# Performance work log

Hardware: AMD Instinct MI355X
Metric: run time of the kernel (lower is better)

## Reference

```python
import jax, jax.numpy as jnp
from jax import lax
import numpy as np

B = 2048
NUM_COMPO = 650
NUM_CHARS = 27533
COMPO_SCORE_THRESH = 0.7
SCORE_ADJ_SCALE = 0.1
K = 10  # top-k chars and max padded hit indices


def setup_inputs() -> dict:
    key = jax.random.key(0)
    k1, k2, k3, k4, k5 = jax.random.split(key, 5)
    return {
        "pred_class_logits": jax.random.normal(k1, (B, NUM_CHARS), dtype=jnp.float32),
        "pred_compo_logits": jax.random.normal(k2, (B, NUM_COMPO), dtype=jnp.float32),
        "chinese_char_ids": jax.random.randint(k3, (B,), 0, NUM_CHARS, dtype=jnp.int32),
        "compo_co_occurrence_prob": jax.random.uniform(k4, (NUM_COMPO, NUM_COMPO), dtype=jnp.float32),
        "compo_chinese_matrix": jax.random.randint(k5, (NUM_COMPO, NUM_CHARS), 0, 2, dtype=jnp.int32),
    }


def _components_to_char(compo_scores, co_occ, matrix):
    """Per-sample: compo_scores [C], co_occ [C,C], matrix [C,V] (0/1 int)."""
    # score adjustment: sum over compos with score>0.88 of co_occ row * score * scale
    hi = compo_scores > 0.88
    w = jnp.where(hi, compo_scores, 0.0)                       # [C]
    adjusted = compo_scores + SCORE_ADJ_SCALE * (w @ co_occ)   # [C]
    max_idx = jnp.argmax(adjusted)
    max_score = compo_scores[max_idx]

    # select compos above threshold, sorted descending by score
    sel = compo_scores > COMPO_SCORE_THRESH
    num_sel = jnp.sum(sel.astype(jnp.int32))
    masked = jnp.where(sel, compo_scores, -jnp.inf)
    order = jnp.argsort(-masked)                                # selected first, desc
    sorted_scores = jnp.take(compo_scores, order)               # [C]

    hit0 = matrix[max_idx]                                      # [V] int

    def cond(st):
        i, hit, _prev = st
        return (i < num_sel) & (jnp.sum(hit) > 1)

    def body(st):
        i, hit, _prev = st
        comp = matrix[order[i]]
        new_hit = ((hit + comp) == 2).astype(hit.dtype)         # intersection
        return (i + 1, new_hit, hit)

    i, hit, prev = lax.while_loop(cond, body, (jnp.int32(1), hit0, hit0))
    num_hit = jnp.sum(hit)
    empty = num_hit == 0
    i = jnp.where(empty, i - 1, i)
    hit = jnp.where(empty, prev, hit)
    hit_score = jnp.where(i == 1, max_score, sorted_scores[i - 1])

    # first K indices where hit == 1, padded with -1 (fixed shape)
    ar = jnp.arange(NUM_CHARS, dtype=jnp.int32)
    vals = jnp.where(hit == 1, NUM_CHARS - ar, 0)
    topv, topi = lax.top_k(vals, K)
    hit_indices = jnp.where(topv > 0, topi.astype(jnp.int32), -1)
    return adjusted, hit_indices, hit_score


def reference(pred_class_logits, pred_compo_logits, chinese_char_ids,
              compo_co_occurrence_prob, compo_chinese_matrix):
    class_probs = jax.nn.softmax(pred_class_logits, axis=1)     # [B, V]
    compo_scores = jax.nn.sigmoid(pred_compo_logits)            # [B, C]
    class_scores, class_indices = lax.top_k(class_probs, K)     # [B, K]

    adjusted, hit_idx, hit_scores = jax.vmap(
        _components_to_char, in_axes=(0, None, None)
    )(compo_scores, compo_co_occurrence_prob, compo_chinese_matrix)

    num_hit = jnp.sum((hit_idx != -1).astype(jnp.int32), axis=1)  # [B]
    pred1 = jnp.where(num_hit == 1, hit_idx[:, 0], class_indices[:, 0])
    pred2 = jnp.where((class_scores[:, 0] < 0.85) & (num_hit == 1),
                      hit_idx[:, 0], class_indices[:, 0])

    hit_compare = jnp.any(class_indices[:, :, None] == hit_idx[:, None, :], axis=2)  # [B,K]
    j = jnp.argmax(hit_compare, axis=1)  # first True (all-False -> 0), matches stable desc argsort[0]
    pred3 = class_indices[jnp.arange(class_indices.shape[0]), j]

    return (class_indices, class_scores, compo_scores, adjusted,
            hit_idx, hit_scores, pred1, pred2, pred3)
```

## Files before the change

kernel.cpp:

```cpp
#include <hip/hip_runtime.h>
#include <math.h>

#define NB 2048
#define NC 650
#define NV 27533
#define NK 10
#define NWRD 861
#define NT 256
#define NCHUNK 11
#define SVCAP 768
#define T0 2.5f

__global__ __launch_bounds__(NT) void pack_kernel(const int* __restrict__ mat,
                                                  unsigned* __restrict__ packed) {
  const int c = blockIdx.x;
  __shared__ unsigned s_w[NWRD];
  for (int w = threadIdx.x; w < NWRD; w += NT) s_w[w] = 0;
  __syncthreads();
  const size_t rbeg = (size_t)c * NV;
  const size_t g0 = rbeg & ~(size_t)3;
  const int pre = (int)(rbeg - g0);
  const int nchunks = (NV + pre + 3) >> 2;
  const size_t NTOT = (size_t)NC * NV;
  for (int t = threadIdx.x; t < nchunks; t += NT) {
    size_t g = g0 + ((size_t)t << 2);
    int4 q;
    if (g + 4 <= NTOT) {
      q = *(const int4*)(mat + g);
    } else {
      q.x = (g < NTOT) ? mat[g] : 0;
      q.y = (g + 1 < NTOT) ? mat[g + 1] : 0;
      q.z = (g + 2 < NTOT) ? mat[g + 2] : 0;
      q.w = (g + 3 < NTOT) ? mat[g + 3] : 0;
    }
    long e0 = (long)g - (long)rbeg;
    unsigned nib = 0;
    if (q.x && e0 >= 0 && e0 < NV) nib |= 1u;
    if (q.y && e0 + 1 >= 0 && e0 + 1 < NV) nib |= 2u;
    if (q.z && e0 + 2 >= 0 && e0 + 2 < NV) nib |= 4u;
    if (q.w && e0 + 3 >= 0 && e0 + 3 < NV) nib |= 8u;
    if (nib) {
      if (e0 < 0) { nib >>= (int)(-e0); e0 = 0; }
      int w = (int)(e0 >> 5), sh = (int)(e0 & 31);
      unsigned long long m = (unsigned long long)nib << sh;
      atomicOr(&s_w[w], (unsigned)m);
      unsigned hi = (unsigned)(m >> 32);
      if (hi && w + 1 < NWRD) atomicOr(&s_w[w + 1], hi);
    }
  }
  __syncthreads();
  unsigned* orow = packed + (size_t)c * NWRD;
  for (int w = threadIdx.x; w < NWRD; w += NT) orow[w] = s_w[w];
}

__global__ __launch_bounds__(NT, 6) void gen_pred_kernel(
    const float* __restrict__ class_logits,
    const float* __restrict__ compo_logits,
    const float* __restrict__ co_occ,
    const unsigned* __restrict__ packed,
    float* __restrict__ out) {
  const int b = blockIdx.x;
  const int tid = threadIdx.x;
  const int lane = tid & 63;
  const int wid = tid >> 6;

  __shared__ __align__(16) char arena[10464];
  float* s_sv_v = (float*)arena;
  int* s_sv_i = (int*)(arena + 3072);
  float* s_score = (float*)arena;
  int* s_selidx = (int*)(arena + 2608);
  int* s_hi = (int*)(arena + 5216);
  int* s_order = (int*)(arena + 7824);
  __shared__ unsigned s_words[NWRD];

  __shared__ float red_f[4];
  __shared__ float red_s[4];
  __shared__ int red_i[4];
  __shared__ int s_svcnt, s_cnt, s_i;
  __shared__ int s_cls_idx[NK];
  __shared__ float s_cls_sc[NK];
  __shared__ int s_hit[NK];
  __shared__ int s_hicnt[NCHUNK];
  __shared__ int s_selcnt[NCHUNK];

  const size_t o_cidx = 0;
  const size_t o_csc = (size_t)NB * NK;
  const size_t o_comp = 2 * (size_t)NB * NK;
  const size_t o_adj = o_comp + (size_t)NB * NC;
  const size_t o_hidx = o_adj + (size_t)NB * NC;
  const size_t o_hsc = o_hidx + (size_t)NB * NK;
  const size_t o_p1 = o_hsc + NB;
  const size_t o_p2 = o_p1 + NB;
  const size_t o_p3 = o_p2 + NB;

  const float* lg = class_logits + (size_t)b * NV;
  const int s0 = (4 - (b & 3)) & 3;
  const int M4 = (NV - s0) >> 2;
  const int baseT = s0 + (M4 << 2);
  const float4* lg4 = (const float4*)(lg + s0);

  if (tid == 0) s_svcnt = 0;
  __syncthreads();

  float mx = -INFINITY, ss0 = 0.f, ss1 = 0.f;

#define APPEND1(x, e)                                                   \
  { int p_ = atomicAdd(&s_svcnt, 1);                                    \
    if (p_ < SVCAP) { s_sv_v[p_] = (x); s_sv_i[p_] = (e); } }

  if (tid < s0) {
    float x = lg[tid];
    ss0 += __expf(x); mx = fmaxf(mx, x);
    if (x >= T0) APPEND1(x, tid);
  }
  {
    int rem = NV - baseT;
    if (tid < rem) {
      float x = lg[baseT + tid];
      ss1 += __expf(x); mx = fmaxf(mx, x);
      if (x >= T0) APPEND1(x, baseT + tid);
    }
  }

#define PROC4(f, ebase)                                                  \
  {                                                                      \
    ss0 += __expf(f.x); ss1 += __expf(f.y);                              \
    ss0 += __expf(f.z); ss1 += __expf(f.w);                              \
    float m4_ = fmaxf(fmaxf(f.x, f.y), fmaxf(f.z, f.w));                 \
    mx = fmaxf(mx, m4_);                                                 \
    if (m4_ >= T0) {                                                     \
      int e_ = (ebase);                                                  \
      int c_ = (f.x >= T0) + (f.y >= T0) + (f.z >= T0) + (f.w >= T0);    \
      int p_ = atomicAdd(&s_svcnt, c_);                                  \
      if (f.x >= T0) { if (p_ < SVCAP) { s_sv_v[p_] = f.x; s_sv_i[p_] = e_; } p_++; }     \
      if (f.y >= T0) { if (p_ < SVCAP) { s_sv_v[p_] = f.y; s_sv_i[p_] = e_ + 1; } p_++; } \
      if (f.z >= T0) { if (p_ < SVCAP) { s_sv_v[p_] = f.z; s_sv_i[p_] = e_ + 2; } p_++; } \
      if (f.w >= T0) { if (p_ < SVCAP) { s_sv_v[p_] = f.w; s_sv_i[p_] = e_ + 3; } p_++; } \
    }                                                                    \
  }

  {
    int v = tid;
    float4 fa, fb;
    bool hb = (v + NT) < M4;
    if (v < M4) fa = lg4[v];
    if (hb) fb = lg4[v + NT];
    while (v < M4) {
      int va = v + 2 * NT, vb = v + 3 * NT;
      float4 fa2, fb2;
      bool ha2 = va < M4, hb2 = vb < M4;
      if (ha2) fa2 = lg4[va];
      if (hb2) fb2 = lg4[vb];
      PROC4(fa, s0 + (v << 2));
      if (hb) PROC4(fb, s0 + ((v + NT) << 2));
      fa = fa2; fb = fb2; hb = hb2; v = va;
    }
  }

  {
    float s = ss0 + ss1;
#pragma unroll
    for (int off = 32; off > 0; off >>= 1) s += __shfl_down(s, off);
    float g = mx;
    g = fmaxf(g, __shfl_xor(g, 1));
    g = fmaxf(g, __shfl_xor(g, 2));
    g = fmaxf(g, __shfl_xor(g, 4));
    g = fmaxf(g, __shfl_xor(g, 8));
    float t = fminf(g, __shfl_xor(g, 16));
    t = fminf(t, __shfl_xor(t, 32));
    if (lane == 0) { red_s[wid] = s; red_f[wid] = t; }
  }
  __syncthreads();
  const float Sv = red_s[0] + red_s[1] + red_s[2] + red_s[3];
  const float T = fminf(fminf(red_f[0], red_f[1]), fminf(red_f[2], red_f[3]));
  int svc = s_svcnt;

  if (svc < NK || svc > SVCAP) {
    __syncthreads();
    if (tid == 0) s_svcnt = 0;
    __syncthreads();
    if (tid < s0) { float x = lg[tid]; if (x >= T) APPEND1(x, tid); }
    {
      int rem = NV - baseT;
      if (tid < rem) { float x = lg[baseT + tid]; if (x >= T) APPEND1(x, baseT + tid); }
    }
    for (int v = tid; v < M4; v += NT) {
      float4 f = lg4[v];
      int e = s0 + (v << 2);
      if (f.x >= T) APPEND1(f.x, e);
      if (f.y >= T) APPEND1(f.y, e + 1);
      if (f.z >= T) APPEND1(f.z, e + 2);
      if (f.w >= T) APPEND1(f.w, e + 3);
    }
    __syncthreads();
    svc = s_svcnt;
  }
#undef APPEND1
#undef PROC4
  __syncthreads();

  {
    int S = svc < SVCAP ? svc : SVCAP;
    for (int t2 = tid; t2 < S; t2 += NT) {
      float vt = s_sv_v[t2];
      int it = s_sv_i[t2];
      int r = 0;
      for (int q = 0; q < S; q++) {
        float vq = s_sv_v[q];
        int iq = s_sv_i[q];
        r += (vq > vt || (vq == vt && iq < it)) ? 1 : 0;
      }
      if (r < NK) { s_cls_idx[r] = it; s_cls_sc[r] = vt; }
    }
  }
  __syncthreads();
  if (tid < NK) {
    int cidx = s_cls_idx[tid];
    float sc = __expf(s_cls_sc[tid]) / Sv;
    s_cls_sc[tid] = sc;
    out[o_cidx + (size_t)b * NK + tid] = (float)cidx;
    out[o_csc + (size_t)b * NK + tid] = sc;
  }

  const float* cl = compo_logits + (size_t)b * NC;
  for (int j = tid; j < NC; j += NT) {
    float x = cl[j];
    float sc = 1.f / (1.f + expf(-x));
    s_score[j] = sc;
    out[o_comp + (size_t)b * NC + j] = sc;
  }
  __syncthreads();

  for (int c = wid; c < NCHUNK; c += 4) {
    int e = (c << 6) + lane;
    float s = (e < NC) ? s_score[e] : 0.f;
    unsigned long long mh = __ballot(s > 0.88f);
    unsigned long long ms = __ballot(s > 0.7f);
    if (lane == 0) { s_hicnt[c] = __popcll(mh); s_selcnt[c] = __popcll(ms); }
  }
  __syncthreads();
  int nhi = 0, nsel = 0;
#pragma unroll
  for (int q = 0; q < NCHUNK; q++) { nhi += s_hicnt[q]; nsel += s_selcnt[q]; }
  for (int c = wid; c < NCHUNK; c += 4) {
    int e = (c << 6) + lane;
    float s = (e < NC) ? s_score[e] : 0.f;
    unsigned long long mh = __ballot(s > 0.88f);
    unsigned long long ms = __ballot(s > 0.7f);
    int oh = 0, os = 0;
    for (int q = 0; q < c; q++) { oh += s_hicnt[q]; os += s_selcnt[q]; }
    unsigned long long lower = (1ull << lane) - 1ull;
    if (s > 0.88f) s_hi[oh + __popcll(mh & lower)] = e;
    if (s > 0.7f) s_selidx[os + __popcll(ms & lower)] = e;
  }
  __syncthreads();

  for (int t = tid; t < nsel; t += NT) {
    int j = s_selidx[t];
    float sj = s_score[j];
    int r = 0;
    for (int q = 0; q < nsel; q++) {
      int jq = s_selidx[q];
      float sq = s_score[jq];
      r += (sq > sj || (sq == sj && jq < j)) ? 1 : 0;
    }
    s_order[r] = j;
  }

  float bestv = -INFINITY;
  int besti = 0x7fffffff;
  for (int j = tid; j < NC; j += NT) {
    float a0 = 0.f, a1 = 0.f, a2 = 0.f, a3 = 0.f;
    int h = 0;
    for (; h + 4 <= nhi; h += 4) {
      int i0 = s_hi[h], i1 = s_hi[h + 1], i2 = s_hi[h + 2], i3 = s_hi[h + 3];
      float c0 = co_occ[(size_t)i0 * NC + j];
      float c1 = co_occ[(size_t)i1 * NC + j];
      float c2 = co_occ[(size_t)i2 * NC + j];
      float c3 = co_occ[(size_t)i3 * NC + j];
      a0 = fmaf(s_score[i0], c0, a0);
      a1 = fmaf(s_score[i1], c1, a1);
      a2 = fmaf(s_score[i2], c2, a2);
      a3 = fmaf(s_score[i3], c3, a3);
    }
    for (; h < nhi; h++) {
      int ih = s_hi[h];
      a0 = fmaf(s_score[ih], co_occ[(size_t)ih * NC + j], a0);
    }
    float adj = s_score[j] + 0.1f * ((a0 + a1) + (a2 + a3));
    out[o_adj + (size_t)b * NC + j] = adj;
    if (adj > bestv || (adj == bestv && j < besti)) { bestv = adj; besti = j; }
  }
#pragma unroll
  for (int off = 32; off > 0; off >>= 1) {
    float ov = __shfl_down(bestv, off);
    int oi = __shfl_down(besti, off);
    if (ov > bestv || (ov == bestv && oi < besti)) { bestv = ov; besti = oi; }
  }
  if (lane == 0) { red_f[wid] = bestv; red_i[wid] = besti; }
  __syncthreads();
  int max_idx;
  {
    float bv = red_f[0]; int bi = red_i[0];
#pragma unroll
    for (int q = 1; q < 4; q++) {
      float qv = red_f[q]; int qi = red_i[q];
      if (qv > bv || (qv == bv && qi < bi)) { bv = qv; bi = qi; }
    }
    max_idx = bi;
  }
  const float max_score = s_score[max_idx];
  __syncthreads();

  if (wid == 0) {
    unsigned hw[14], pf[14];
    const unsigned* prow = packed + (size_t)max_idx * NWRD;
    int pc = 0;
#pragma unroll
    for (int t = 0; t < 14; t++) {
      int w = (t << 6) + lane;
      unsigned x = (w < NWRD) ? prow[w] : 0u;
      hw[t] = x;
      pc += __popc(x);
    }
#pragma unroll
    for (int off = 32; off > 0; off >>= 1) pc += __shfl_down(pc, off);
    int cnt = __shfl(pc, 0);
    int i = 1;
    if (nsel > 1) {
      const unsigned* row = packed + (size_t)s_order[1] * NWRD;
#pragma unroll
      for (int t = 0; t < 14; t++) {
        int w = (t << 6) + lane;
        pf[t] = (w < NWRD) ? row[w] : 0u;
      }
    }
    while (i < nsel && cnt > 1) {
      int p2 = 0;
#pragma unroll
      for (int t = 0; t < 14; t++) p2 += __popc(hw[t] & pf[t]);
#pragma unroll
      for (int off = 32; off > 0; off >>= 1) p2 += __shfl_down(p2, off);
      int np = __shfl(p2, 0);
      if (np == 0) break;
#pragma unroll
      for (int t = 0; t < 14; t++) hw[t] &= pf[t];
      cnt = np;
      i++;
      if (i < nsel) {
        const unsigned* row = packed + (size_t)s_order[i] * NWRD;
#pragma unroll
        for (int t = 0; t < 14; t++) {
          int w = (t << 6) + lane;
          pf[t] = (w < NWRD) ? row[w] : 0u;
        }
      }
    }
#pragma unroll
    for (int t = 0; t < 14; t++) {
      int w = (t << 6) + lane;
      if (w < NWRD) s_words[w] = hw[t];
    }
    if (lane == 0) { s_cnt = cnt; s_i = i; }
  }
  __syncthreads();

  if (tid < NK) s_hit[tid] = -1;
  {
    unsigned wv[4];
    int myc = 0;
#pragma unroll
    for (int t = 0; t < 4; t++) {
      int w = (tid << 2) + t;
      unsigned x = (w < NWRD) ? s_words[w] : 0u;
      wv[t] = x;
      myc += __popc(x);
    }
    int inc = myc;
#pragma unroll
    for (int off = 1; off < 64; off <<= 1) {
      int y = __shfl_up(inc, off);
      if (lane >= off) inc += y;
    }
    if (lane == 63) red_i[wid] = inc;
    __syncthreads();
    int excl = inc - myc;
    for (int q = 0; q < wid; q++) excl += red_i[q];
    int r = excl;
    if (r < NK) {
#pragma unroll
      for (int t = 0; t < 4; t++) {
        unsigned x = wv[t];
        int wb = ((tid << 2) + t) << 5;
        while (x && r < NK) {
          int bpos = __ffs(x) - 1;
          x &= x - 1;
          s_hit[r] = wb + bpos;
          r++;
        }
        if (r >= NK) break;
      }
    }
  }
  __syncthreads();

  {
    int cnt = s_cnt, i = s_i;
    int num_hit = cnt < NK ? cnt : NK;
    if (tid < NK) out[o_hidx + (size_t)b * NK + tid] = (float)s_hit[tid];
    if (tid == 0) {
      float hsc = (i <= 1) ? max_score : s_score[s_order[i - 1]];
      out[o_hsc + b] = hsc;
      int ci0 = s_cls_idx[0];
      float cs0 = s_cls_sc[0];
      int h0 = s_hit[0];
      int p1 = (num_hit == 1) ? h0 : ci0;
      int p2 = (cs0 < 0.85f && num_hit == 1) ? h0 : ci0;
      int jj = 0;
      for (int k = 0; k < NK; k++) {
        bool m = false;
#pragma unroll
        for (int q = 0; q < NK; q++) m = m || (s_cls_idx[k] == s_hit[q]);
        if (m) { jj = k; break; }
      }
      out[o_p1 + b] = (float)p1;
      out[o_p2 + b] = (float)p2;
      out[o_p3 + b] = (float)s_cls_idx[jj];
    }
  }
}

extern "C" void kernel_launch(void* const* d_in, const int* in_sizes, int n_in,
                              void* d_out, int out_size, void* d_ws, size_t ws_size,
                              hipStream_t stream) {
  const float* class_logits = (const float*)d_in[0];
  const float* compo_logits = (const float*)d_in[1];
  const float* co_occ = (const float*)d_in[3];
  const int* mat = (const int*)d_in[4];
  float* out = (float*)d_out;
  unsigned* packed = (unsigned*)d_ws;

  pack_kernel<<<NC, NT, 0, stream>>>(mat, packed);
  gen_pred_kernel<<<NB, NT, 0, stream>>>(class_logits, compo_logits, co_occ,
                                         packed, out);
}
```

Baseline: 450.2 us.

## Prefetch two rows ahead in intersection loop, shrink top-k candidate buffer, cache scores

The hit-intersection loop now prefetches packed rows two iterations ahead and replaces the full popcount reduction with ballot-based checks for 'more than one hit'. The top-k candidate threshold is raised and its buffer shrunk. Shared memory is repartitioned to cut LDS use, and selected and high scores are stored next to their indices so inner loops avoid indirect lookups. Compo logits are loaded early to hide their latency. The higher threshold risks more fallback passes when too few candidates pass it.

Measured after the change: 422.2 us. -6.2%, faster.

```diff
diff --git a/kernel.cpp b/kernel.cpp
--- a/kernel.cpp
+++ b/kernel.cpp
@@ -8,8 +8,8 @@
 #define NWRD 861
 #define NT 256
 #define NCHUNK 11
-#define SVCAP 768
-#define T0 2.5f
+#define SVCAP 512
+#define T0 2.8f
 
 __global__ __launch_bounds__(NT) void pack_kernel(const int* __restrict__ mat,
                                                   unsigned* __restrict__ packed) {
@@ -64,19 +64,22 @@
   const int lane = tid & 63;
   const int wid = tid >> 6;
 
-  __shared__ __align__(16) char arena[10464];
+  __shared__ __align__(16) char arena[7808];
   float* s_sv_v = (float*)arena;
-  int* s_sv_i = (int*)(arena + 3072);
+  int* s_sv_i = (int*)(arena + 2048);
   float* s_score = (float*)arena;
-  int* s_selidx = (int*)(arena + 2608);
-  int* s_hi = (int*)(arena + 5216);
-  int* s_order = (int*)(arena + 7824);
-  __shared__ unsigned s_words[NWRD];
+  int* s_selidx = (int*)(arena + 2600);
+  float* s_selsc = (float*)(arena + 5200);
+  __shared__ __align__(16) char arena2[5200];
+  int* s_hi = (int*)arena2;
+  float* s_hisc = (float*)(arena2 + 2600);
+  unsigned* s_words = (unsigned*)arena2;
+  __shared__ int s_order[NC];
 
   __shared__ float red_f[4];
   __shared__ float red_s[4];
   __shared__ int red_i[4];
-  __shared__ int s_svcnt, s_cnt, s_i;
+  __shared__ int s_svcnt, s_i;
   __shared__ int s_cls_idx[NK];
   __shared__ float s_cls_sc[NK];
   __shared__ int s_hit[NK];
@@ -157,6 +160,14 @@
     }
   }
 
+  float cl0 = 0.f, cl1 = 0.f, cl2 = 0.f;
+  {
+    const float* cl = compo_logits + (size_t)b * NC;
+    if (tid < NC) cl0 = cl[tid];
+    if (tid + NT < NC) cl1 = cl[tid + NT];
+    if (tid + 2 * NT < NC) cl2 = cl[tid + 2 * NT];
+  }
+
   {
     float s = ss0 + ss1;
 #pragma unroll
@@ -205,6 +216,7 @@
       float vt = s_sv_v[t2];
       int it = s_sv_i[t2];
       int r = 0;
+#pragma unroll 8
       for (int q = 0; q < S; q++) {
         float vq = s_sv_v[q];
         int iq = s_sv_i[q];
@@ -222,12 +234,20 @@
     out[o_csc + (size_t)b * NK + tid] = sc;
   }
 
-  const float* cl = compo_logits + (size_t)b * NC;
-  for (int j = tid; j < NC; j += NT) {
-    float x = cl[j];
-    float sc = 1.f / (1.f + expf(-x));
-    s_score[j] = sc;
-    out[o_comp + (size_t)b * NC + j] = sc;
+  if (tid < NC) {
+    float sc = 1.f / (1.f + expf(-cl0));
+    s_score[tid] = sc;
+    out[o_comp + (size_t)b * NC + tid] = sc;
+  }
+  if (tid + NT < NC) {
+    float sc = 1.f / (1.f + expf(-cl1));
+    s_score[tid + NT] = sc;
+    out[o_comp + (size_t)b * NC + tid + NT] = sc;
+  }
+  if (tid + 2 * NT < NC) {
+    float sc = 1.f / (1.f + expf(-cl2));
+    s_score[tid + 2 * NT] = sc;
+    out[o_comp + (size_t)b * NC + tid + 2 * NT] = sc;
   }
   __syncthreads();
 
@@ -250,21 +270,26 @@
     int oh = 0, os = 0;
     for (int q = 0; q < c; q++) { oh += s_hicnt[q]; os += s_selcnt[q]; }
     unsigned long long lower = (1ull << lane) - 1ull;
-    if (s > 0.88f) s_hi[oh + __popcll(mh & lower)] = e;
-    if (s > 0.7f) s_selidx[os + __popcll(ms & lower)] = e;
+    if (s > 0.88f) {
+      int p = oh + __popcll(mh & lower);
+      s_hi[p] = e; s_hisc[p] = s;
+    }
+    if (s > 0.7f) {
+      int p = os + __popcll(ms & lower);
+      s_selidx[p] = e; s_selsc[p] = s;
+    }
   }
   __syncthreads();
 
   for (int t = tid; t < nsel; t += NT) {
-    int j = s_selidx[t];
-    float sj = s_score[j];
+    float sj = s_selsc[t];
     int r = 0;
+#pragma unroll 8
     for (int q = 0; q < nsel; q++) {
-      int jq = s_selidx[q];
-      float sq = s_score[jq];
-      r += (sq > sj || (sq == sj && jq < j)) ? 1 : 0;
-    }
-    s_order[r] = j;
+      float sq = s_selsc[q];
+      r += (sq > sj || (sq == sj && q < t)) ? 1 : 0;
+    }
+    s_order[r] = s_selidx[t];
   }
 
   float bestv = -INFINITY;
@@ -274,18 +299,19 @@
     int h = 0;
     for (; h + 4 <= nhi; h += 4) {
       int i0 = s_hi[h], i1 = s_hi[h + 1], i2 = s_hi[h + 2], i3 = s_hi[h + 3];
+      float w0 = s_hisc[h], w1 = s_hisc[h + 1];
+      float w2 = s_hisc[h + 2], w3 = s_hisc[h + 3];
       float c0 = co_occ[(size_t)i0 * NC + j];
       float c1 = co_occ[(size_t)i1 * NC + j];
       float c2 = co_occ[(size_t)i2 * NC + j];
       float c3 = co_occ[(size_t)i3 * NC + j];
-      a0 = fmaf(s_score[i0], c0, a0);
-      a1 = fmaf(s_score[i1], c1, a1);
-      a2 = fmaf(s_score[i2], c2, a2);
-      a3 = fmaf(s_score[i3], c3, a3);
+      a0 = fmaf(w0, c0, a0);
+      a1 = fmaf(w1, c1, a1);
+      a2 = fmaf(w2, c2, a2);
+      a3 = fmaf(w3, c3, a3);
     }
     for (; h < nhi; h++) {
-      int ih = s_hi[h];
-      a0 = fmaf(s_score[ih], co_occ[(size_t)ih * NC + j], a0);
+      a0 = fmaf(s_hisc[h], co_occ[(size_t)s_hi[h] * NC + j], a0);
     }
     float adj = s_score[j] + 0.1f * ((a0 + a1) + (a2 + a3));
     out[o_adj + (size_t)b * NC + j] = adj;
@@ -313,7 +339,7 @@
   __syncthreads();
 
   if (wid == 0) {
-    unsigned hw[14], pf[14];
+    unsigned hw[14], pf0[14], pf1[14];
     const unsigned* prow = packed + (size_t)max_idx * NWRD;
     int pc = 0;
 #pragma unroll
@@ -323,36 +349,43 @@
       hw[t] = x;
       pc += __popc(x);
     }
-#pragma unroll
-    for (int off = 32; off > 0; off >>= 1) pc += __shfl_down(pc, off);
-    int cnt = __shfl(pc, 0);
+    unsigned long long nz0 = __ballot(pc != 0);
+    bool many = (__ballot(pc > 1) != 0ull) || (__popcll(nz0) > 1);
     int i = 1;
     if (nsel > 1) {
       const unsigned* row = packed + (size_t)s_order[1] * NWRD;
 #pragma unroll
       for (int t = 0; t < 14; t++) {
         int w = (t << 6) + lane;
-        pf[t] = (w < NWRD) ? row[w] : 0u;
-      }
-    }
-    while (i < nsel && cnt > 1) {
+        pf0[t] = (w < NWRD) ? row[w] : 0u;
+      }
+    }
+    if (nsel > 2) {
+      const unsigned* row = packed + (size_t)s_order[2] * NWRD;
+#pragma unroll
+      for (int t = 0; t < 14; t++) {
+        int w = (t << 6) + lane;
+        pf1[t] = (w < NWRD) ? row[w] : 0u;
+      }
+    }
+    while (i < nsel && many) {
       int p2 = 0;
 #pragma unroll
-      for (int t = 0; t < 14; t++) p2 += __popc(hw[t] & pf[t]);
-#pragma unroll
-      for (int off = 32; off > 0; off >>= 1) p2 += __shfl_down(p2, off);
-      int np = __shfl(p2, 0);
-      if (np == 0) break;
-#pragma unroll
-      for (int t = 0; t < 14; t++) hw[t] &= pf[t];
-      cnt = np;
+      for (int t = 0; t < 14; t++) p2 += __popc(hw[t] & pf0[t]);
+      unsigned long long bnz = __ballot(p2 != 0);
+      if (bnz == 0ull) break;
+#pragma unroll
+      for (int t = 0; t < 14; t++) hw[t] &= pf0[t];
+      many = (__ballot(p2 > 1) != 0ull) || (__popcll(bnz) > 1);
       i++;
-      if (i < nsel) {
-        const unsigned* row = packed + (size_t)s_order[i] * NWRD;
+#pragma unroll
+      for (int t = 0; t < 14; t++) pf0[t] = pf1[t];
+      if (i + 1 < nsel && many) {
+        const unsigned* row = packed + (size_t)s_order[i + 1] * NWRD;
 #pragma unroll
         for (int t = 0; t < 14; t++) {
           int w = (t << 6) + lane;
-          pf[t] = (w < NWRD) ? row[w] : 0u;
+          pf1[t] = (w < NWRD) ? row[w] : 0u;
         }
       }
     }
@@ -361,7 +394,7 @@
       int w = (t << 6) + lane;
       if (w < NWRD) s_words[w] = hw[t];
     }
-    if (lane == 0) { s_cnt = cnt; s_i = i; }
+    if (lane == 0) s_i = i;
   }
   __syncthreads();
 
@@ -405,8 +438,7 @@
   __syncthreads();
 
   {
-    int cnt = s_cnt, i = s_i;
-    int num_hit = cnt < NK ? cnt : NK;
+    int i = s_i;
     if (tid < NK) out[o_hidx + (size_t)b * NK + tid] = (float)s_hit[tid];
     if (tid == 0) {
       float hsc = (i <= 1) ? max_score : s_score[s_order[i - 1]];
@@ -414,8 +446,9 @@
       int ci0 = s_cls_idx[0];
       float cs0 = s_cls_sc[0];
       int h0 = s_hit[0];
-      int p1 = (num_hit == 1) ? h0 : ci0;
-      int p2 = (cs0 < 0.85f && num_hit == 1) ? h0 : ci0;
+      bool nh1 = (s_hit[0] >= 0) && (s_hit[1] < 0);
+      int p1 = nh1 ? h0 : ci0;
+      int p2 = (cs0 < 0.85f && nh1) ? h0 : ci0;
       int jj = 0;
       for (int k = 0; k < NK; k++) {
         bool m = false;
```
